# Kernel tuning notes

Hardware: AMD Instinct MI355X
Metric: run time of the kernel (lower is better)

## Reference

```python
import jax, jax.numpy as jnp
import numpy as np

B, S, D, H = 4, 2048, 1024, 16
HD = D // H  # head_dim = 64


def setup_inputs() -> dict:
    key = jax.random.key(0)
    ks = jax.random.split(key, 6)
    scale = 0.02
    x = jax.random.normal(ks[0], (B, S, D), dtype=jnp.float32)
    # per-head projection weights, torch Linear is y = x @ W.T; store as [H, D, HD]
    Wq = jax.random.normal(ks[1], (H, D, HD), dtype=jnp.float32) * scale
    Wk = jax.random.normal(ks[2], (H, D, HD), dtype=jnp.float32) * scale
    Wv = jax.random.normal(ks[3], (H, D, HD), dtype=jnp.float32) * scale
    Wo = jax.random.normal(ks[4], (D, D), dtype=jnp.float32) * scale  # torch [out, in]
    bo = jax.random.normal(ks[5], (D,), dtype=jnp.float32) * scale
    return {"x": x, "Wq": Wq, "Wk": Wk, "Wv": Wv, "Wo": Wo, "bo": bo}


def reference(x, Wq, Wk, Wv, Wo, bo):
    # project: [B,S,D] x [H,D,HD] -> [B,H,S,HD]
    q = jnp.einsum("bsd,hde->bhse", x, Wq)
    k = jnp.einsum("bsd,hde->bhse", x, Wk)
    v = jnp.einsum("bsd,hde->bhse", x, Wv)
    scores = jnp.einsum("bhse,bhte->bhst", q, k) / jnp.sqrt(jnp.float32(HD))
    causal = jnp.tril(jnp.ones((S, S), dtype=bool))  # same as registered tril mask
    scores = jnp.where(causal, scores, -jnp.inf)
    w = jax.nn.softmax(scores, axis=-1)
    out = jnp.einsum("bhst,bhte->bhse", w, v)  # [B,H,S,HD]
    # concat heads along feature dim: [B,S,H*HD] = [B,S,D]
    out = out.transpose(0, 2, 1, 3).reshape(B, S, D)
    # output projection: torch Linear y = x @ W.T + b
    return jnp.einsum("bsd,od->bso", out, Wo) + bo
```

## Files before the change

kernel.cpp:

```cpp
#include <hip/hip_runtime.h>
#include <hip/hip_bf16.h>

typedef __bf16 bf16x8 __attribute__((ext_vector_type(8)));
typedef float f32x4 __attribute__((ext_vector_type(4)));
typedef unsigned short u16x4 __attribute__((ext_vector_type(4)));
typedef unsigned short u16x8 __attribute__((ext_vector_type(8)));
typedef unsigned uint4v __attribute__((ext_vector_type(4)));

#define B_ 4
#define S_ 2048
#define D_ 1024
#define H_ 16
#define HD_ 64

__device__ __forceinline__ unsigned short f2bf(float f) {
  unsigned u = __float_as_uint(f);
  u += 0x7fff + ((u >> 16) & 1);
  return (unsigned short)(u >> 16);
}

__device__ __forceinline__ void gload16(const void* g, void* l) {
  __builtin_amdgcn_global_load_lds((const __attribute__((address_space(1))) unsigned int*)g,
                                   (__attribute__((address_space(3))) unsigned int*)l,
                                   16, 0, 0);
}

__global__ void pack_x_k(const float* __restrict__ in, unsigned short* __restrict__ out, int n4) {
  int i = blockIdx.x * blockDim.x + threadIdx.x;
  int stride = gridDim.x * blockDim.x;
  for (; i < n4; i += stride) {
    float4 v = reinterpret_cast<const float4*>(in)[i];
    u16x4 o = {f2bf(v.x), f2bf(v.y), f2bf(v.z), f2bf(v.w)};
    reinterpret_cast<u16x4*>(out)[i] = o;
  }
}

__global__ void pack_wqkv_k(const float* __restrict__ Wq, const float* __restrict__ Wk,
                            const float* __restrict__ Wv, unsigned short* __restrict__ Wt) {
  int o = blockIdx.x * blockDim.x + threadIdx.x;
  int n = o >> 10;
  int d = o & 1023;
  const float* W = (n < 1024) ? Wq : (n < 2048) ? Wk : Wv;
  int nn = n & 1023;
  int h = nn >> 6, e = nn & 63;
  Wt[o] = f2bf(W[(h << 16) + (d << 6) + e]);
}

__global__ __launch_bounds__(512, 2) void gemm256_k(const unsigned short* __restrict__ A,
                                                    const unsigned short* __restrict__ Bt,
                                                    unsigned short* __restrict__ C,
                                                    int M, int N, int K) {
  __shared__ __align__(16) unsigned short lds[2][2][2][128 * 64];
  const int tid = threadIdx.x;
  const int wid = tid >> 6, lane = tid & 63;
  const int r = lane & 15, g = lane >> 4;
  const int wm = wid >> 2, wn = wid & 3;

  const int i_hw = blockIdx.y * gridDim.x + blockIdx.x;
  const int xcd = i_hw & 7, j = i_hw >> 3;
  const long arow0 = (long)((xcd & 3) * 8 + (j & 7)) * 256;
  const long bcol0 = (long)((xcd >> 2) * 6 + (j >> 3)) * 256;

  const f32x4 z4 = {0.f, 0.f, 0.f, 0.f};
  f32x4 acc[8][4];
#pragma unroll
  for (int m = 0; m < 8; ++m)
#pragma unroll
    for (int n = 0; n < 4; ++n) acc[m][n] = z4;

  auto stage_half = [&](int kt, int op, int h) {
    const unsigned short* src = op ? Bt + (bcol0 + 128 * h) * K : A + (arow0 + 128 * h) * K;
    const int k0 = kt << 6;
    unsigned short* base = &lds[kt & 1][op][h][0];
#pragma unroll
    for (int c = 0; c < 2; ++c) {
      const int jj = c * 512 + (wid << 6) + lane;
      const int row = jj >> 3, cc = jj & 7;
      const int ccs = cc ^ (row & 7);
      gload16(src + (long)row * K + k0 + ccs * 8, base + (c * 512 + (wid << 6)) * 8);
    }
  };

  bf16x8 af[4][2], bv0[2][2], bv1[2][2];
  auto read_a = [&](int buf, int mh) {
#pragma unroll
    for (int i2 = 0; i2 < 4; ++i2)
#pragma unroll
      for (int kk = 0; kk < 2; ++kk) {
        const int rowh = (2 * i2 + wm) * 16 + r;
        af[i2][kk] = *(const bf16x8*)&lds[buf][0][mh][rowh * 64 + (((kk << 2) + g) ^ (rowh & 7)) * 8];
      }
  };
  auto read_b = [&](bf16x8 (&bv)[2][2], int buf, int nh) {
#pragma unroll
    for (int j2 = 0; j2 < 2; ++j2)
#pragma unroll
      for (int kk = 0; kk < 2; ++kk) {
        const int rowh = (4 * j2 + wn) * 16 + r;
        bv[j2][kk] = *(const bf16x8*)&lds[buf][1][nh][rowh * 64 + (((kk << 2) + g) ^ (rowh & 7)) * 8];
      }
  };
  auto mma_q = [&](bf16x8 (&bv)[2][2], int mh, int nh) {
    __builtin_amdgcn_s_setprio(1);
#pragma unroll
    for (int kk = 0; kk < 2; ++kk)
#pragma unroll
      for (int i2 = 0; i2 < 4; ++i2)
#pragma unroll
        for (int j2 = 0; j2 < 2; ++j2)
          acc[4 * mh + i2][2 * nh + j2] = __builtin_amdgcn_mfma_f32_16x16x32_bf16(
              af[i2][kk], bv[j2][kk], acc[4 * mh + i2][2 * nh + j2], 0, 0, 0);
    __builtin_amdgcn_s_setprio(0);
  };

  const int nk = K >> 6;
  stage_half(0, 0, 0);
  stage_half(0, 1, 0);
  stage_half(0, 1, 1);
  stage_half(0, 0, 1);
  asm volatile("s_waitcnt vmcnt(4)" ::: "memory");
  asm volatile("s_barrier" ::: "memory");

  for (int t = 0; t < nk; ++t) {
    const int buf = t & 1;
    const bool pre = (t + 1 < nk);
    read_a(buf, 0);
    read_b(bv0, buf, 0);
    if (pre) { stage_half(t + 1, 0, 0); stage_half(t + 1, 1, 0); }
    asm volatile("s_barrier" ::: "memory");
    mma_q(bv0, 0, 0);
    if (pre) asm volatile("s_waitcnt vmcnt(6)" ::: "memory");
    else     asm volatile("s_waitcnt vmcnt(2)" ::: "memory");
    asm volatile("s_waitcnt lgkmcnt(0)\n\ts_barrier" ::: "memory");
    read_b(bv1, buf, 1);
    if (pre) stage_half(t + 1, 1, 1);
    asm volatile("s_barrier" ::: "memory");
    mma_q(bv1, 0, 1);
    if (pre) asm volatile("s_waitcnt vmcnt(6)" ::: "memory");
    else     asm volatile("s_waitcnt vmcnt(0)" ::: "memory");
    asm volatile("s_waitcnt lgkmcnt(0)\n\ts_barrier" ::: "memory");
    read_a(buf, 1);
    if (pre) stage_half(t + 1, 0, 1);
    asm volatile("s_barrier" ::: "memory");
    mma_q(bv1, 1, 1);
    asm volatile("s_waitcnt lgkmcnt(0)\n\ts_barrier" ::: "memory");
    asm volatile("s_barrier" ::: "memory");
    mma_q(bv0, 1, 0);
    if (pre) asm volatile("s_waitcnt vmcnt(4)" ::: "memory");
    asm volatile("s_waitcnt lgkmcnt(0)\n\ts_barrier" ::: "memory");
  }

#pragma unroll
  for (int m = 0; m < 8; ++m)
#pragma unroll
    for (int n = 0; n < 4; ++n)
#pragma unroll
      for (int rr = 0; rr < 4; ++rr) {
        const long row = arow0 + (2 * m + wm) * 16 + g * 4 + rr;
        const long col = bcol0 + (4 * n + wn) * 16 + r;
        C[row * N + col] = f2bf(acc[m][n][rr]);
      }
}

__global__ __launch_bounds__(256, 2) void gemm_bt_k(const unsigned short* __restrict__ A,
                                                    const unsigned short* __restrict__ Bt,
                                                    float* __restrict__ C,
                                                    const float* __restrict__ bias,
                                                    int M, int N, int K) {
  __shared__ __align__(16) unsigned short lA[2][128 * 64];
  __shared__ __align__(16) unsigned short lB[2][128 * 64];
  const int tid = threadIdx.x;
  const int wid = tid >> 6, lane = tid & 63;
  const int r = lane & 15, g = lane >> 4;
  const long arow0 = (long)blockIdx.x * 128;
  const long brow0 = (long)blockIdx.y * 128;
  const int wr = (wid >> 1) * 64, wc = (wid & 1) * 64;

  const f32x4 z4 = {0.f, 0.f, 0.f, 0.f};
  f32x4 acc[4][4];
#pragma unroll
  for (int m = 0; m < 4; ++m)
#pragma unroll
    for (int n = 0; n < 4; ++n) acc[m][n] = z4;

  auto stage = [&](int buf, int k0) {
#pragma unroll
    for (int c = 0; c < 4; ++c) {
      const int j = c * 256 + wid * 64 + lane;
      const int row = j >> 3, col = (j & 7) * 8;
      gload16(A + (arow0 + row) * K + k0 + col, &lA[buf][(c * 256 + wid * 64) * 8]);
      gload16(Bt + (brow0 + row) * K + k0 + col, &lB[buf][(c * 256 + wid * 64) * 8]);
    }
  };

  stage(0, 0);
  __syncthreads();
  const int nk = K >> 6;
  for (int kt = 0; kt < nk; ++kt) {
    const int cur = kt & 1;
    if (kt + 1 < nk) stage(cur ^ 1, (kt + 1) << 6);
#pragma unroll
    for (int kk = 0; kk < 2; ++kk) {
      bf16x8 af[4], bfr[4];
#pragma unroll
      for (int m = 0; m < 4; ++m)
        af[m] = *(const bf16x8*)&lA[cur][(wr + m * 16 + r) * 64 + kk * 32 + g * 8];
#pragma unroll
      for (int n = 0; n < 4; ++n)
        bfr[n] = *(const bf16x8*)&lB[cur][(wc + n * 16 + r) * 64 + kk * 32 + g * 8];
#pragma unroll
      for (int m = 0; m < 4; ++m)
#pragma unroll
        for (int n = 0; n < 4; ++n)
          acc[m][n] = __builtin_amdgcn_mfma_f32_16x16x32_bf16(af[m], bfr[n], acc[m][n], 0, 0, 0);
    }
    __syncthreads();
  }

#pragma unroll
  for (int m = 0; m < 4; ++m) {
#pragma unroll
    for (int n = 0; n < 4; ++n) {
#pragma unroll
      for (int rr = 0; rr < 4; ++rr) {
        const long row = arow0 + wr + m * 16 + g * 4 + rr;
        const long col = brow0 + wc + n * 16 + r;
        C[row * N + col] = acc[m][n][rr] + bias[col];
      }
    }
  }
}

__global__ __launch_bounds__(256, 2) void attn_k(const unsigned short* __restrict__ qkv,
                                                 unsigned short* __restrict__ out) {
  __shared__ __align__(16) unsigned short lK[2][64 * 64];
  __shared__ __align__(16) unsigned short lVt[2][64 * 64];

  const int tid = threadIdx.x, wid = tid >> 6, lane = tid & 63;
  const int r = lane & 15, g = lane >> 4;
  const int bh = blockIdx.x;
  const int b = bh >> 4, h = bh & 15;
  const int qb = 15 - (int)blockIdx.y;
  const int q0 = qb * 128;

  const long base = ((long)b * S_) * 3072 + h * 64;
  const unsigned short* Qg = qkv + base;
  const unsigned short* Kg = qkv + base + 1024;
  const unsigned short* Vg = qkv + base + 2048;

  int qrow[2];
  bf16x8 qf[2][2];
#pragma unroll
  for (int qs = 0; qs < 2; ++qs) {
    qrow[qs] = q0 + qs * 64 + wid * 16 + r;
#pragma unroll
    for (int kk = 0; kk < 2; ++kk)
      qf[qs][kk] = *(const bf16x8*)&Qg[(long)qrow[qs] * 3072 + kk * 32 + g * 8];
  }

  const f32x4 z4 = {0.f, 0.f, 0.f, 0.f};
  f32x4 o[2][4];
#pragma unroll
  for (int qs = 0; qs < 2; ++qs)
#pragma unroll
    for (int nt = 0; nt < 4; ++nt) o[qs][nt] = z4;
  float m_i[2] = {-1e30f, -1e30f};
  float l_i[2] = {0.f, 0.f};

  u16x8 kreg[2], vreg[2];
  auto load_regs = [&](int t0) {
#pragma unroll
    for (int c = 0; c < 2; ++c) {
      const int j = c * 256 + tid;
      const int tt = j >> 3, e0 = (j & 7) * 8;
      kreg[c] = *(const u16x8*)&Kg[(long)(t0 + tt) * 3072 + e0];
      const int tc = j & 63, ec = j >> 6;
      vreg[c] = *(const u16x8*)&Vg[(long)(t0 + tc) * 3072 + ec * 8];
    }
  };
  auto write_lds = [&](int buf) {
#pragma unroll
    for (int c = 0; c < 2; ++c) {
      const int j = c * 256 + tid;
      const int row = j >> 3, cc = j & 7;
      *(u16x8*)&lK[buf][(row * 8 + (cc ^ (row & 7))) * 8] = kreg[c];
      const int tc = j & 63, ec = j >> 6;
#pragma unroll
      for (int i = 0; i < 8; ++i) {
        const int e = ec * 8 + i;
        lVt[buf][e * 64 + (tc ^ (i * 8))] = vreg[c][i];
      }
    }
  };

  const int ntiles = (q0 >> 6) + 2;
  load_regs(0);
  write_lds(0);

  for (int t = 0; t < ntiles; ++t) {
    const int cur = t & 1;
    if (t + 1 < ntiles) load_regs((t + 1) << 6);
    __syncthreads();

    const int t0 = t << 6;
    const bool act0 = (t < ntiles - 1);
    const bool diag0 = (t == ntiles - 2);
    const bool diag1 = (t == ntiles - 1);

    f32x4 st[2][4];
#pragma unroll
    for (int tt = 0; tt < 4; ++tt) { st[0][tt] = z4; st[1][tt] = z4; }
    __builtin_amdgcn_s_setprio(1);
#pragma unroll
    for (int kk = 0; kk < 2; ++kk)
#pragma unroll
      for (int tt = 0; tt < 4; ++tt) {
        const int row = tt * 16 + r, cc = kk * 4 + g;
        bf16x8 kf = *(const bf16x8*)&lK[cur][(row * 8 + (cc ^ (row & 7))) * 8];
        st[1][tt] = __builtin_amdgcn_mfma_f32_16x16x32_bf16(kf, qf[1][kk], st[1][tt], 0, 0, 0);
        if (act0)
          st[0][tt] = __builtin_amdgcn_mfma_f32_16x16x32_bf16(kf, qf[0][kk], st[0][tt], 0, 0, 0);
      }
    __builtin_amdgcn_s_setprio(0);

    bf16x8 pf[2][2];
    unsigned corr_bits[2] = {0x3f800000u, 0x3f800000u};
    bool dodef[2] = {true, true};
#pragma unroll
    for (int qs = 0; qs < 2; ++qs) {
      if (qs == 0 && !act0) continue;
      const bool diag = qs ? diag1 : diag0;
      float sv[16];
#pragma unroll
      for (int tt = 0; tt < 4; ++tt)
#pragma unroll
        for (int rg = 0; rg < 4; ++rg) {
          float s = st[qs][tt][rg];
          if (diag && (t0 + tt * 16 + g * 4 + rg > qrow[qs])) s = -1e30f;
          sv[tt * 4 + rg] = s;
        }
      float h0 = fmaxf(fmaxf(fmaxf(sv[0], sv[1]), fmaxf(sv[2], sv[3])),
                       fmaxf(fmaxf(sv[4], sv[5]), fmaxf(sv[6], sv[7])));
      float h1 = fmaxf(fmaxf(fmaxf(sv[8], sv[9]), fmaxf(sv[10], sv[11])),
                       fmaxf(fmaxf(sv[12], sv[13]), fmaxf(sv[14], sv[15])));
      const float pmax = fmaxf(h0, h1);
      const bool defer = __all(pmax - m_i[qs] <= 64.f);
      float corr = 1.f;
      if (!defer) {
        float mx = fmaxf(pmax, m_i[qs]);
        mx = fmaxf(mx, __shfl_xor(mx, 16, 64));
        mx = fmaxf(mx, __shfl_xor(mx, 32, 64));
        corr = __expf((m_i[qs] - mx) * 0.125f);
        m_i[qs] = mx;
      }
      dodef[qs] = defer;
      corr_bits[qs] = __float_as_uint(corr);
      const float m8 = m_i[qs] * 0.125f;
      float p[16];
      float rs = 0.f;
#pragma unroll
      for (int i = 0; i < 16; ++i) {
        p[i] = __expf(__builtin_fmaf(sv[i], 0.125f, -m8));
        rs += p[i];
      }
      rs += __shfl_xor(rs, 16, 64);
      rs += __shfl_xor(rs, 32, 64);
      l_i[qs] = l_i[qs] * corr + rs;
      unsigned cw[4][2];
#pragma unroll
      for (int tt = 0; tt < 4; ++tt)
#pragma unroll
        for (int e = 0; e < 2; ++e)
          asm("v_cvt_pk_bf16_f32 %0, %1, %2"
              : "=v"(cw[tt][e]) : "v"(p[tt * 4 + 2 * e]), "v"(p[tt * 4 + 2 * e + 1]));
#pragma unroll
      for (int kk = 0; kk < 2; ++kk) {
        unsigned x0 = cw[2 * kk][0], y0 = cw[2 * kk + 1][0];
        unsigned x1 = cw[2 * kk][1], y1 = cw[2 * kk + 1][1];
        asm volatile("v_permlane32_swap_b32 %0, %1" : "+v"(x0), "+v"(y0));
        asm volatile("v_permlane16_swap_b32 %0, %1" : "+v"(x0), "+v"(y0));
        asm volatile("v_permlane32_swap_b32 %0, %1" : "+v"(x1), "+v"(y1));
        asm volatile("v_permlane16_swap_b32 %0, %1" : "+v"(x1), "+v"(y1));
        uint4v w = {x0, x1, y0, y1};
        pf[qs][kk] = *(bf16x8*)&w;
      }
    }
#pragma unroll
    for (int qs = 0; qs < 2; ++qs) {
      if (qs == 0 && !act0) continue;
      if (!dodef[qs]) {
        const float corr = __uint_as_float(corr_bits[qs]);
#pragma unroll
        for (int rr = 0; rr < 4; ++rr) {
          const float c = __shfl(corr, g * 4 + rr, 64);
#pragma unroll
          for (int nt = 0; nt < 4; ++nt) o[qs][nt][rr] *= c;
        }
      }
    }

    __builtin_amdgcn_s_setprio(1);
#pragma unroll
    for (int kk = 0; kk < 2; ++kk)
#pragma unroll
      for (int nt = 0; nt < 4; ++nt) {
        const int row = nt * 16 + r, cc = kk * 4 + g;
        const bf16x8 vf = *(const bf16x8*)&lVt[cur][(row * 8 + (cc ^ (row & 7))) * 8];
        o[1][nt] = __builtin_amdgcn_mfma_f32_16x16x32_bf16(pf[1][kk], vf, o[1][nt], 0, 0, 0);
        if (act0)
          o[0][nt] = __builtin_amdgcn_mfma_f32_16x16x32_bf16(pf[0][kk], vf, o[0][nt], 0, 0, 0);
      }
    __builtin_amdgcn_s_setprio(0);

    if (t + 1 < ntiles) write_lds(cur ^ 1);
  }

#pragma unroll
  for (int qs = 0; qs < 2; ++qs) {
    float linv[4];
#pragma unroll
    for (int rr = 0; rr < 4; ++rr)
      linv[rr] = 1.f / __shfl(l_i[qs], g * 4 + rr, 64);
#pragma unroll
    for (int nt = 0; nt < 4; ++nt)
#pragma unroll
      for (int rr = 0; rr < 4; ++rr) {
        const long s = q0 + qs * 64 + wid * 16 + g * 4 + rr;
        out[((long)b * S_ + s) * 1024 + h * 64 + nt * 16 + r] = f2bf(o[qs][nt][rr] * linv[rr]);
      }
  }
}

extern "C" void kernel_launch(void* const* d_in, const int* in_sizes, int n_in,
                              void* d_out, int out_size, void* d_ws, size_t ws_size,
                              hipStream_t stream) {
  const float* x = (const float*)d_in[0];
  const float* Wq = (const float*)d_in[1];
  const float* Wk = (const float*)d_in[2];
  const float* Wv = (const float*)d_in[3];
  const float* Wo = (const float*)d_in[4];
  const float* bo = (const float*)d_in[5];
  float* out = (float*)d_out;

  char* ws = (char*)d_ws;
  unsigned short* Xb = (unsigned short*)(ws);
  unsigned short* Wt = (unsigned short*)(ws + (16ul << 20));
  unsigned short* Wob = (unsigned short*)(ws + (22ul << 20));
  unsigned short* QKV = (unsigned short*)(ws + (24ul << 20));
  unsigned short* AO = (unsigned short*)(ws + (72ul << 20));

  pack_x_k<<<2048, 256, 0, stream>>>(x, Xb, (B_ * S_ * D_) / 4);
  pack_x_k<<<512, 256, 0, stream>>>(Wo, Wob, (D_ * D_) / 4);
  pack_wqkv_k<<<(3 * D_ * D_) / 256, 256, 0, stream>>>(Wq, Wk, Wv, Wt);

  gemm256_k<<<dim3(32, 12), 512, 0, stream>>>(Xb, Wt, QKV, B_ * S_, 3 * D_, D_);
  attn_k<<<dim3(64, 16), 256, 0, stream>>>(QKV, AO);
  gemm_bt_k<<<dim3(64, 8), 256, 0, stream>>>(AO, Wob, out, bo, B_ * S_, D_, D_);
}
```

Measured before the change: 187.8 us.

## Shrink QKV GEMM tile to 256x128 and raise attention occupancy hint

The QKV projection GEMM moves from 256x256 output tiles to 256x128 tiles, doubling the grid to 768 blocks. Its LDS staging and pipeline schedule are restructured around a single B half per k-step, with two MFMA phases instead of four. The aim is better CU fill and lower LDS and register pressure, at the cost of less operand reuse per tile. Separately, the attention kernel's launch-bounds hint goes from 2 to 3 blocks per CU, which may force register spilling.

```diff
diff --git a/kernel.cpp b/kernel.cpp
--- a/kernel.cpp
+++ b/kernel.cpp
@@ -50,7 +50,7 @@
                                                     const unsigned short* __restrict__ Bt,
                                                     unsigned short* __restrict__ C,
                                                     int M, int N, int K) {
-  __shared__ __align__(16) unsigned short lds[2][2][2][128 * 64];
+  __shared__ __align__(16) unsigned short lds[2][3][128 * 64];
   const int tid = threadIdx.x;
   const int wid = tid >> 6, lane = tid & 63;
   const int r = lane & 15, g = lane >> 4;
@@ -59,48 +59,48 @@
   const int i_hw = blockIdx.y * gridDim.x + blockIdx.x;
   const int xcd = i_hw & 7, j = i_hw >> 3;
   const long arow0 = (long)((xcd & 3) * 8 + (j & 7)) * 256;
-  const long bcol0 = (long)((xcd >> 2) * 6 + (j >> 3)) * 256;
+  const long bcol0 = (long)((xcd >> 2) * 12 + (j >> 3)) * 128;
 
   const f32x4 z4 = {0.f, 0.f, 0.f, 0.f};
-  f32x4 acc[8][4];
+  f32x4 acc[8][2];
 #pragma unroll
   for (int m = 0; m < 8; ++m)
 #pragma unroll
-    for (int n = 0; n < 4; ++n) acc[m][n] = z4;
-
-  auto stage_half = [&](int kt, int op, int h) {
-    const unsigned short* src = op ? Bt + (bcol0 + 128 * h) * K : A + (arow0 + 128 * h) * K;
+    for (int n = 0; n < 2; ++n) acc[m][n] = z4;
+
+  auto stage_half = [&](int kt, int which) {
+    const unsigned short* src = (which == 2) ? Bt + bcol0 * K : A + (arow0 + 128 * which) * K;
     const int k0 = kt << 6;
-    unsigned short* base = &lds[kt & 1][op][h][0];
+    unsigned short* base = &lds[kt & 1][which][0];
 #pragma unroll
     for (int c = 0; c < 2; ++c) {
-      const int jj = c * 512 + (wid << 6) + lane;
+      const int jj = c * 512 + tid;
       const int row = jj >> 3, cc = jj & 7;
       const int ccs = cc ^ (row & 7);
-      gload16(src + (long)row * K + k0 + ccs * 8, base + (c * 512 + (wid << 6)) * 8);
-    }
-  };
-
-  bf16x8 af[4][2], bv0[2][2], bv1[2][2];
+      gload16(src + (long)row * K + k0 + ccs * 8, base + jj * 8);
+    }
+  };
+
+  bf16x8 af[4][2], bv[2][2];
   auto read_a = [&](int buf, int mh) {
 #pragma unroll
     for (int i2 = 0; i2 < 4; ++i2)
 #pragma unroll
       for (int kk = 0; kk < 2; ++kk) {
         const int rowh = (2 * i2 + wm) * 16 + r;
-        af[i2][kk] = *(const bf16x8*)&lds[buf][0][mh][rowh * 64 + (((kk << 2) + g) ^ (rowh & 7)) * 8];
-      }
-  };
-  auto read_b = [&](bf16x8 (&bv)[2][2], int buf, int nh) {
+        af[i2][kk] = *(const bf16x8*)&lds[buf][mh][rowh * 64 + (((kk << 2) + g) ^ (rowh & 7)) * 8];
+      }
+  };
+  auto read_b = [&](int buf) {
 #pragma unroll
     for (int j2 = 0; j2 < 2; ++j2)
 #pragma unroll
       for (int kk = 0; kk < 2; ++kk) {
         const int rowh = (4 * j2 + wn) * 16 + r;
-        bv[j2][kk] = *(const bf16x8*)&lds[buf][1][nh][rowh * 64 + (((kk << 2) + g) ^ (rowh & 7)) * 8];
-      }
-  };
-  auto mma_q = [&](bf16x8 (&bv)[2][2], int mh, int nh) {
+        bv[j2][kk] = *(const bf16x8*)&lds[buf][2][rowh * 64 + (((kk << 2) + g) ^ (rowh & 7)) * 8];
+      }
+  };
+  auto mma_h = [&](int mh) {
     __builtin_amdgcn_s_setprio(1);
 #pragma unroll
     for (int kk = 0; kk < 2; ++kk)
@@ -108,52 +108,41 @@
       for (int i2 = 0; i2 < 4; ++i2)
 #pragma unroll
         for (int j2 = 0; j2 < 2; ++j2)
-          acc[4 * mh + i2][2 * nh + j2] = __builtin_amdgcn_mfma_f32_16x16x32_bf16(
-              af[i2][kk], bv[j2][kk], acc[4 * mh + i2][2 * nh + j2], 0, 0, 0);
+          acc[4 * mh + i2][j2] = __builtin_amdgcn_mfma_f32_16x16x32_bf16(
+              af[i2][kk], bv[j2][kk], acc[4 * mh + i2][j2], 0, 0, 0);
     __builtin_amdgcn_s_setprio(0);
   };
 
   const int nk = K >> 6;
-  stage_half(0, 0, 0);
-  stage_half(0, 1, 0);
-  stage_half(0, 1, 1);
-  stage_half(0, 0, 1);
-  asm volatile("s_waitcnt vmcnt(4)" ::: "memory");
+  stage_half(0, 0);
+  stage_half(0, 2);
+  stage_half(0, 1);
+  asm volatile("s_waitcnt vmcnt(2)" ::: "memory");
   asm volatile("s_barrier" ::: "memory");
 
   for (int t = 0; t < nk; ++t) {
     const int buf = t & 1;
     const bool pre = (t + 1 < nk);
     read_a(buf, 0);
-    read_b(bv0, buf, 0);
-    if (pre) { stage_half(t + 1, 0, 0); stage_half(t + 1, 1, 0); }
+    read_b(buf);
+    if (pre) { stage_half(t + 1, 0); stage_half(t + 1, 2); }
     asm volatile("s_barrier" ::: "memory");
-    mma_q(bv0, 0, 0);
-    if (pre) asm volatile("s_waitcnt vmcnt(6)" ::: "memory");
-    else     asm volatile("s_waitcnt vmcnt(2)" ::: "memory");
-    asm volatile("s_waitcnt lgkmcnt(0)\n\ts_barrier" ::: "memory");
-    read_b(bv1, buf, 1);
-    if (pre) stage_half(t + 1, 1, 1);
-    asm volatile("s_barrier" ::: "memory");
-    mma_q(bv1, 0, 1);
-    if (pre) asm volatile("s_waitcnt vmcnt(6)" ::: "memory");
+    mma_h(0);
+    if (pre) asm volatile("s_waitcnt vmcnt(4)" ::: "memory");
     else     asm volatile("s_waitcnt vmcnt(0)" ::: "memory");
     asm volatile("s_waitcnt lgkmcnt(0)\n\ts_barrier" ::: "memory");
     read_a(buf, 1);
-    if (pre) stage_half(t + 1, 0, 1);
+    if (pre) stage_half(t + 1, 1);
     asm volatile("s_barrier" ::: "memory");
-    mma_q(bv1, 1, 1);
+    mma_h(1);
+    if (pre) asm volatile("s_waitcnt vmcnt(2)" ::: "memory");
     asm volatile("s_waitcnt lgkmcnt(0)\n\ts_barrier" ::: "memory");
-    asm volatile("s_barrier" ::: "memory");
-    mma_q(bv0, 1, 0);
-    if (pre) asm volatile("s_waitcnt vmcnt(4)" ::: "memory");
-    asm volatile("s_waitcnt lgkmcnt(0)\n\ts_barrier" ::: "memory");
   }
 
 #pragma unroll
   for (int m = 0; m < 8; ++m)
 #pragma unroll
-    for (int n = 0; n < 4; ++n)
+    for (int n = 0; n < 2; ++n)
 #pragma unroll
       for (int rr = 0; rr < 4; ++rr) {
         const long row = arow0 + (2 * m + wm) * 16 + g * 4 + rr;
@@ -231,7 +220,7 @@
   }
 }
 
-__global__ __launch_bounds__(256, 2) void attn_k(const unsigned short* __restrict__ qkv,
+__global__ __launch_bounds__(256, 3) void attn_k(const unsigned short* __restrict__ qkv,
                                                  unsigned short* __restrict__ out) {
   __shared__ __align__(16) unsigned short lK[2][64 * 64];
   __shared__ __align__(16) unsigned short lVt[2][64 * 64];
@@ -453,7 +442,7 @@
   pack_x_k<<<512, 256, 0, stream>>>(Wo, Wob, (D_ * D_) / 4);
   pack_wqkv_k<<<(3 * D_ * D_) / 256, 256, 0, stream>>>(Wq, Wk, Wv, Wt);
 
-  gemm256_k<<<dim3(32, 12), 512, 0, stream>>>(Xb, Wt, QKV, B_ * S_, 3 * D_, D_);
+  gemm256_k<<<dim3(32, 24), 512, 0, stream>>>(Xb, Wt, QKV, B_ * S_, 3 * D_, D_);
   attn_k<<<dim3(64, 16), 256, 0, stream>>>(QKV, AO);
   gemm_bt_k<<<dim3(64, 8), 256, 0, stream>>>(AO, Wob, out, bo, B_ * S_, D_, D_);
 }
```

Result: slower. 194.5 us (+3.5%).

## Emit transposed V from QKV GEMM and stage K/V via direct global-to-LDS loads

Applied to the files above, without the earlier changes.

The QKV projection GEMM now writes Q and K into a packed [B*S,2048] buffer and V already transposed per head as [B,H,64,S]. The attention kernel can then stage K and V^T tiles with async global_load_lds copies, dropping the register round trip and the scalar per-element V transpose into LDS. Staging for the next tile is issued right after the barrier, so the copy overlaps compute. The cost is a strided epilogue in the GEMM for the V columns, which may be less coalesced.

```diff
diff --git a/kernel.cpp b/kernel.cpp
--- a/kernel.cpp
+++ b/kernel.cpp
@@ -48,7 +48,8 @@
 
 __global__ __launch_bounds__(512, 2) void gemm256_k(const unsigned short* __restrict__ A,
                                                     const unsigned short* __restrict__ Bt,
-                                                    unsigned short* __restrict__ C,
+                                                    unsigned short* __restrict__ QK,
+                                                    unsigned short* __restrict__ VT,
                                                     int M, int N, int K) {
   __shared__ __align__(16) unsigned short lds[2][2][2][128 * 64];
   const int tid = threadIdx.x;
@@ -150,16 +151,33 @@
     asm volatile("s_waitcnt lgkmcnt(0)\n\ts_barrier" ::: "memory");
   }
 
-#pragma unroll
-  for (int m = 0; m < 8; ++m)
-#pragma unroll
-    for (int n = 0; n < 4; ++n)
-#pragma unroll
-      for (int rr = 0; rr < 4; ++rr) {
-        const long row = arow0 + (2 * m + wm) * 16 + g * 4 + rr;
-        const long col = bcol0 + (4 * n + wn) * 16 + r;
-        C[row * N + col] = f2bf(acc[m][n][rr]);
-      }
+  if (bcol0 < 2048) {
+#pragma unroll
+    for (int m = 0; m < 8; ++m)
+#pragma unroll
+      for (int n = 0; n < 4; ++n)
+#pragma unroll
+        for (int rr = 0; rr < 4; ++rr) {
+          const long row = arow0 + (2 * m + wm) * 16 + g * 4 + rr;
+          const long col = bcol0 + (4 * n + wn) * 16 + r;
+          QK[row * 2048 + col] = f2bf(acc[m][n][rr]);
+        }
+  } else {
+#pragma unroll
+    for (int m = 0; m < 8; ++m) {
+      const long row0 = arow0 + (2 * m + wm) * 16 + g * 4;
+      const long b = row0 >> 11, s = row0 & 2047;
+#pragma unroll
+      for (int n = 0; n < 4; ++n) {
+        const long vcol = bcol0 - 2048 + (4 * n + wn) * 16 + r;
+        const long h = vcol >> 6, e = vcol & 63;
+        u16x4 w4;
+#pragma unroll
+        for (int rr = 0; rr < 4; ++rr) w4[rr] = f2bf(acc[m][n][rr]);
+        *(u16x4*)&VT[(((b << 4) + h) * 64 + e) * 2048 + s] = w4;
+      }
+    }
+  }
 }
 
 __global__ __launch_bounds__(256, 2) void gemm_bt_k(const unsigned short* __restrict__ A,
@@ -231,7 +249,8 @@
   }
 }
 
-__global__ __launch_bounds__(256, 2) void attn_k(const unsigned short* __restrict__ qkv,
+__global__ __launch_bounds__(256, 2) void attn_k(const unsigned short* __restrict__ qk,
+                                                 const unsigned short* __restrict__ vt,
                                                  unsigned short* __restrict__ out) {
   __shared__ __align__(16) unsigned short lK[2][64 * 64];
   __shared__ __align__(16) unsigned short lVt[2][64 * 64];
@@ -243,10 +262,9 @@
   const int qb = 15 - (int)blockIdx.y;
   const int q0 = qb * 128;
 
-  const long base = ((long)b * S_) * 3072 + h * 64;
-  const unsigned short* Qg = qkv + base;
-  const unsigned short* Kg = qkv + base + 1024;
-  const unsigned short* Vg = qkv + base + 2048;
+  const unsigned short* Qg = qk + ((long)b * S_) * 2048 + h * 64;
+  const unsigned short* Kg = Qg + 1024;
+  const unsigned short* Vg = vt + ((long)(b * 16 + h)) * 64 * 2048;
 
   int qrow[2];
   bf16x8 qf[2][2];
@@ -255,7 +273,7 @@
     qrow[qs] = q0 + qs * 64 + wid * 16 + r;
 #pragma unroll
     for (int kk = 0; kk < 2; ++kk)
-      qf[qs][kk] = *(const bf16x8*)&Qg[(long)qrow[qs] * 3072 + kk * 32 + g * 8];
+      qf[qs][kk] = *(const bf16x8*)&Qg[(long)qrow[qs] * 2048 + kk * 32 + g * 8];
   }
 
   const f32x4 z4 = {0.f, 0.f, 0.f, 0.f};
@@ -267,40 +285,24 @@
   float m_i[2] = {-1e30f, -1e30f};
   float l_i[2] = {0.f, 0.f};
 
-  u16x8 kreg[2], vreg[2];
-  auto load_regs = [&](int t0) {
-#pragma unroll
-    for (int c = 0; c < 2; ++c) {
-      const int j = c * 256 + tid;
-      const int tt = j >> 3, e0 = (j & 7) * 8;
-      kreg[c] = *(const u16x8*)&Kg[(long)(t0 + tt) * 3072 + e0];
-      const int tc = j & 63, ec = j >> 6;
-      vreg[c] = *(const u16x8*)&Vg[(long)(t0 + tc) * 3072 + ec * 8];
-    }
-  };
-  auto write_lds = [&](int buf) {
+  auto stage = [&](int buf, int t0) {
 #pragma unroll
     for (int c = 0; c < 2; ++c) {
       const int j = c * 256 + tid;
       const int row = j >> 3, cc = j & 7;
-      *(u16x8*)&lK[buf][(row * 8 + (cc ^ (row & 7))) * 8] = kreg[c];
-      const int tc = j & 63, ec = j >> 6;
-#pragma unroll
-      for (int i = 0; i < 8; ++i) {
-        const int e = ec * 8 + i;
-        lVt[buf][e * 64 + (tc ^ (i * 8))] = vreg[c][i];
-      }
+      const int ccs = (cc ^ (row & 7)) << 3;
+      gload16(Kg + (long)(t0 + row) * 2048 + ccs, &lK[buf][j * 8]);
+      gload16(Vg + (long)row * 2048 + t0 + ccs, &lVt[buf][j * 8]);
     }
   };
 
   const int ntiles = (q0 >> 6) + 2;
-  load_regs(0);
-  write_lds(0);
+  stage(0, 0);
 
   for (int t = 0; t < ntiles; ++t) {
     const int cur = t & 1;
-    if (t + 1 < ntiles) load_regs((t + 1) << 6);
     __syncthreads();
+    if (t + 1 < ntiles) stage(cur ^ 1, (t + 1) << 6);
 
     const int t0 = t << 6;
     const bool act0 = (t < ntiles - 1);
@@ -411,8 +413,6 @@
           o[0][nt] = __builtin_amdgcn_mfma_f32_16x16x32_bf16(pf[0][kk], vf, o[0][nt], 0, 0, 0);
       }
     __builtin_amdgcn_s_setprio(0);
-
-    if (t + 1 < ntiles) write_lds(cur ^ 1);
   }
 
 #pragma unroll
@@ -446,14 +446,15 @@
   unsigned short* Xb = (unsigned short*)(ws);
   unsigned short* Wt = (unsigned short*)(ws + (16ul << 20));
   unsigned short* Wob = (unsigned short*)(ws + (22ul << 20));
-  unsigned short* QKV = (unsigned short*)(ws + (24ul << 20));
+  unsigned short* QK = (unsigned short*)(ws + (24ul << 20));
+  unsigned short* VT = (unsigned short*)(ws + (56ul << 20));
   unsigned short* AO = (unsigned short*)(ws + (72ul << 20));
 
   pack_x_k<<<2048, 256, 0, stream>>>(x, Xb, (B_ * S_ * D_) / 4);
   pack_x_k<<<512, 256, 0, stream>>>(Wo, Wob, (D_ * D_) / 4);
   pack_wqkv_k<<<(3 * D_ * D_) / 256, 256, 0, stream>>>(Wq, Wk, Wv, Wt);
 
-  gemm256_k<<<dim3(32, 12), 512, 0, stream>>>(Xb, Wt, QKV, B_ * S_, 3 * D_, D_);
-  attn_k<<<dim3(64, 16), 256, 0, stream>>>(QKV, AO);
+  gemm256_k<<<dim3(32, 12), 512, 0, stream>>>(Xb, Wt, QK, VT, B_ * S_, 3 * D_, D_);
+  attn_k<<<dim3(64, 16), 256, 0, stream>>>(QK, VT, AO);
   gemm_bt_k<<<dim3(64, 8), 256, 0, stream>>>(AO, Wob, out, bo, B_ * S_, D_, D_);
 }
```

After: 190.3 us. Within noise of the previous version (+1.3%).
